# Performance work log

Hardware: AMD Instinct MI355X
Metric: run time of the kernel (lower is better)

The kernel has to match this reference:

```python
import jax, jax.numpy as jnp
import numpy as np

N, E, D, H, O, G = 50000, 640000, 128, 128, 16, 64


def setup_inputs() -> dict:
    key = jax.random.key(0)
    ks = jax.random.split(key, 10)
    x = jax.random.normal(ks[0], (N, D), dtype=jnp.float32)
    edge_index = jax.random.randint(ks[1], (2, E), 0, N, dtype=jnp.int64)
    edge_weight = jax.random.uniform(ks[2], (E,), dtype=jnp.float32)
    batch = jnp.sort(jax.random.randint(ks[3], (N,), 0, G, dtype=jnp.int64))
    s1 = 1.0 / np.sqrt(D)
    s2 = 1.0 / np.sqrt(H)
    W1 = jax.random.uniform(ks[4], (D, H), jnp.float32, -s1, s1)
    b1 = jnp.zeros((H,), jnp.float32)
    W2 = jax.random.uniform(ks[5], (H, H), jnp.float32, -s2, s2)
    b2 = jnp.zeros((H,), jnp.float32)
    Wfc = jax.random.uniform(ks[6], (H, O), jnp.float32, -s2, s2)
    bfc = jax.random.uniform(ks[7], (O,), jnp.float32, -s2, s2)
    return dict(x=x, edge_index=edge_index, edge_weight=edge_weight, batch=batch,
                W1=W1, b1=b1, W2=W2, b2=b2, Wfc=Wfc, bfc=bfc)


def _gcn_conv(x, row, col, ew, W, b, n):
    # PyG GCNConv: out[i] = sum_{(j->i)} norm_ji * (x[j] @ W) + b
    xw = x @ W
    deg = jax.ops.segment_sum(ew, col, num_segments=n)          # [N]
    dinv = jnp.where(deg > 0, jax.lax.rsqrt(deg), 0.0)
    norm = dinv[row] * ew * dinv[col]                           # [E+N]
    msg = xw[row] * norm[:, None]                               # gather + scale
    return jax.ops.segment_sum(msg, col, num_segments=n) + b    # scatter-add


def reference(x, edge_index, edge_weight, batch, W1, b1, W2, b2, Wfc, bfc):
    n = x.shape[0]
    # add self-loops with weight 1 (PyG gcn_norm default)
    loop = jnp.arange(n, dtype=edge_index.dtype)
    row = jnp.concatenate([edge_index[0], loop])
    col = jnp.concatenate([edge_index[1], loop])
    ew = jnp.concatenate([edge_weight, jnp.ones((n,), edge_weight.dtype)])

    h = jax.nn.relu(_gcn_conv(x, row, col, ew, W1, b1, n))
    h = jax.nn.relu(_gcn_conv(h, row, col, ew, W2, b2, n))

    # global_mean_pool over graph ids
    sums = jax.ops.segment_sum(h, batch, num_segments=G)        # [G, H]
    cnt = jax.ops.segment_sum(jnp.ones((n,), h.dtype), batch, num_segments=G)
    pooled = sums / jnp.maximum(cnt, 1.0)[:, None]
    return pooled @ Wfc + bfc                                   # [G, O]
```

## Files before the change

### kernel.cpp

```cpp
#include <hip/hip_runtime.h>


typedef _Float16 h4 __attribute__((ext_vector_type(4)));
typedef _Float16 h8 __attribute__((ext_vector_type(8)));
typedef float f32x4 __attribute__((ext_vector_type(4)));

__global__ void rank_kernel(const int* __restrict__ row, const int* __restrict__ col,
                            int* __restrict__ cnt, unsigned short* __restrict__ rank,
                            int E, int C) {
    int e = blockIdx.x * blockDim.x + threadIdx.x;
    if (e >= E) return;
    int key = col[e] * C + (row[e] >> 13);
    rank[e] = (unsigned short)atomicAdd(&cnt[key], 1);
}

__global__ void block_sum_kernel(const int* __restrict__ cnt, int* __restrict__ bsum, int NC) {
    __shared__ int s[512];
    int t = threadIdx.x;
    int i = blockIdx.x * 512 + t;
    s[t] = (i < NC) ? cnt[i] : 0;
    __syncthreads();
    for (int off = 256; off > 0; off >>= 1) {
        if (t < off) s[t] += s[t + off];
        __syncthreads();
    }
    if (t == 0) bsum[blockIdx.x] = s[0];
}

__global__ void scan_bsum_kernel(const int* __restrict__ bsum, int* __restrict__ boff,
                                 int* __restrict__ rowptr, int NC, int nb) {
    __shared__ int s[1024];
    int t = threadIdx.x;
    int v = (t < nb) ? bsum[t] : 0;
    s[t] = v;
    __syncthreads();
    for (int off = 1; off < 1024; off <<= 1) {
        int u = (t >= off) ? s[t - off] : 0;
        __syncthreads();
        s[t] += u;
        __syncthreads();
    }
    if (t < nb) boff[t] = s[t] - v;
    if (t == nb - 1) rowptr[NC] = s[t];
}

__global__ void rowptr_kernel(const int* __restrict__ cnt, const int* __restrict__ boff,
                              int* __restrict__ rowptr, int NC) {
    __shared__ int s[512];
    int t = threadIdx.x;
    int i = blockIdx.x * 512 + t;
    int v = (i < NC) ? cnt[i] : 0;
    s[t] = v;
    __syncthreads();
    for (int off = 1; off < 512; off <<= 1) {
        int u = (t >= off) ? s[t - off] : 0;
        __syncthreads();
        s[t] += u;
        __syncthreads();
    }
    if (i < NC) rowptr[i] = boff[blockIdx.x] + s[t] - v;
}

__global__ void scatter_kernel(const int* __restrict__ row, const int* __restrict__ col,
                               const float* __restrict__ ew,
                               const unsigned short* __restrict__ rank,
                               const int* __restrict__ rowptr,
                               unsigned int* __restrict__ csr, int E, int C) {
    int e = blockIdx.x * blockDim.x + threadIdx.x;
    if (e >= E) return;
    int r = row[e];
    int pos = rowptr[col[e] * C + (r >> 13)] + (int)rank[e];
    unsigned short hw = __builtin_bit_cast(unsigned short, (_Float16)ew[e]);
    csr[pos] = ((unsigned int)r << 16) | (unsigned int)hw;
}

__global__ __launch_bounds__(256) void deginv_convert_kernel(
        const float4* __restrict__ x4, const unsigned int* __restrict__ csr,
        const int* __restrict__ rowptr, float* __restrict__ dinv,
        h4* __restrict__ p16, int n, int C) {
    int node = blockIdx.x * 8 + (threadIdx.x >> 5);
    if (node >= n) return;
    int lane = threadIdx.x & 31;
    int beg = rowptr[node * C], end = rowptr[node * C + C];
    float sum = 0.0f;
    for (int k = beg + lane; k < end; k += 32) {
        unsigned int v = __builtin_nontemporal_load(csr + k);
        sum += (float)__builtin_bit_cast(_Float16, (unsigned short)(v & 0xffffu));
    }
#pragma unroll
    for (int m = 16; m >= 1; m >>= 1) sum += __shfl_xor(sum, m);
    float di = rsqrtf(1.0f + sum);
    if (lane == 0) dinv[node] = di;
    float4 v = x4[(size_t)node * 32 + lane];
    h4 h;
    h.x = (_Float16)(di * v.x); h.y = (_Float16)(di * v.y);
    h.z = (_Float16)(di * v.z); h.w = (_Float16)(di * v.w);
    p16[(size_t)node * 32 + lane] = h;
}

__global__ __launch_bounds__(256) void agg_kernel(const h4* __restrict__ in16,
                                                  const int* __restrict__ rowptr,
                                                  const unsigned int* __restrict__ csr,
                                                  const float* __restrict__ dinv,
                                                  h4* __restrict__ out16, int n, int C) {
    int node = blockIdx.x * 8 + (threadIdx.x >> 5);
    if (node >= n) return;
    int lane = threadIdx.x & 31;
    float di = dinv[node];
    h4 v = in16[(size_t)node * 32 + lane];
    float ax = (float)v.x, ay = (float)v.y, az = (float)v.z, aw = (float)v.w;
    int beg = rowptr[node * C], end = rowptr[node * C + C];
    int idx = beg;
    for (; idx + 4 <= end; idx += 4) {
        unsigned int e0 = __builtin_nontemporal_load(csr + idx + 0);
        unsigned int e1 = __builtin_nontemporal_load(csr + idx + 1);
        unsigned int e2 = __builtin_nontemporal_load(csr + idx + 2);
        unsigned int e3 = __builtin_nontemporal_load(csr + idx + 3);
        h4 u0 = in16[(size_t)(e0 >> 16) * 32 + lane];
        h4 u1 = in16[(size_t)(e1 >> 16) * 32 + lane];
        h4 u2 = in16[(size_t)(e2 >> 16) * 32 + lane];
        h4 u3 = in16[(size_t)(e3 >> 16) * 32 + lane];
        float w0 = (float)__builtin_bit_cast(_Float16, (unsigned short)(e0 & 0xffffu));
        float w1 = (float)__builtin_bit_cast(_Float16, (unsigned short)(e1 & 0xffffu));
        float w2 = (float)__builtin_bit_cast(_Float16, (unsigned short)(e2 & 0xffffu));
        float w3 = (float)__builtin_bit_cast(_Float16, (unsigned short)(e3 & 0xffffu));
        ax += w0 * (float)u0.x; ay += w0 * (float)u0.y; az += w0 * (float)u0.z; aw += w0 * (float)u0.w;
        ax += w1 * (float)u1.x; ay += w1 * (float)u1.y; az += w1 * (float)u1.z; aw += w1 * (float)u1.w;
        ax += w2 * (float)u2.x; ay += w2 * (float)u2.y; az += w2 * (float)u2.z; aw += w2 * (float)u2.w;
        ax += w3 * (float)u3.x; ay += w3 * (float)u3.y; az += w3 * (float)u3.z; aw += w3 * (float)u3.w;
    }
    for (; idx < end; ++idx) {
        unsigned int e0 = __builtin_nontemporal_load(csr + idx);
        float ww = (float)__builtin_bit_cast(_Float16, (unsigned short)(e0 & 0xffffu));
        h4 u = in16[(size_t)(e0 >> 16) * 32 + lane];
        ax += ww * (float)u.x; ay += ww * (float)u.y;
        az += ww * (float)u.z; aw += ww * (float)u.w;
    }
    h4 r;
    r.x = (_Float16)(ax * di); r.y = (_Float16)(ay * di);
    r.z = (_Float16)(az * di); r.w = (_Float16)(aw * di);
    out16[(size_t)node * 32 + lane] = r;
}

__global__ __launch_bounds__(256) void packW_kernel(const float* __restrict__ W1,
                                                    const float* __restrict__ W2,
                                                    _Float16* __restrict__ Wp1,
                                                    _Float16* __restrict__ Wp2) {
    const float* W = blockIdx.x ? W2 : W1;
    _Float16* Wp = blockIdx.x ? Wp2 : Wp1;
    for (int i = threadIdx.x; i < 2048; i += 256) {
        int lane = i & 63, kc = i >> 6;
        int c = kc >> 2, kb = kc & 3;
        int colq = lane & 15, quad = lane >> 4;
        h8 v;
#pragma unroll
        for (int j = 0; j < 8; ++j)
            v[j] = (_Float16)W[(kb * 32 + quad * 8 + j) * 128 + c * 16 + colq];
        ((h8*)Wp)[i] = v;
    }
}

template <int SCALE>
__global__ __launch_bounds__(256) void gemm_mfma(const _Float16* __restrict__ A,
                                                 const h8* __restrict__ Wp,
                                                 const float* __restrict__ bias,
                                                 const float* __restrict__ dinv,
                                                 _Float16* __restrict__ out16, int n) {
    int wid = threadIdx.x >> 6, lane = threadIdx.x & 63;
    int tb = blockIdx.x * 64 + wid * 16;
    if (tb >= n) return;
    int colq = lane & 15, quad = lane >> 4;

    int arow = tb + colq;
    if (arow >= n) arow = n - 1;
    const h8* Arow = (const h8*)(A + (size_t)arow * 128);
    h8 a[4];
#pragma unroll
    for (int kb = 0; kb < 4; ++kb) a[kb] = Arow[kb * 4 + quad];

    f32x4 acc[8];
#pragma unroll
    for (int c = 0; c < 8; ++c) acc[c] = (f32x4)(0.0f);

#pragma unroll
    for (int c = 0; c < 8; ++c) {
#pragma unroll
        for (int kb = 0; kb < 4; ++kb) {
            h8 b = Wp[(c * 4 + kb) * 64 + lane];
            acc[c] = __builtin_amdgcn_mfma_f32_16x16x32_f16(a[kb], b, acc[c], 0, 0, 0);
        }
    }

#pragma unroll
    for (int c = 0; c < 8; ++c) {
        float bz = bias[c * 16 + colq];
#pragma unroll
        for (int r = 0; r < 4; ++r) {
            int row = tb + quad * 4 + r;
            if (row < n) {
                float v = fmaxf(acc[c][r] + bz, 0.0f);
                if (SCALE) v *= dinv[row];
                out16[(size_t)row * 128 + c * 16 + colq] = (_Float16)v;
            }
        }
    }
}

__global__ __launch_bounds__(256) void poolfc_kernel(const h4* __restrict__ h,
                                                     const int* __restrict__ batch,
                                                     const float* __restrict__ Wfc,
                                                     const float* __restrict__ bfc,
                                                     float* __restrict__ out, int n, int O) {
    int g = blockIdx.x;
    __shared__ int sb[2];
    __shared__ float4 red[256];
    __shared__ float pooled[128];
    int t = threadIdx.x;
    if (t < 2) {
        int target = g + t;
        int lo = 0, hi = n;
        while (lo < hi) { int m = (lo + hi) >> 1; if (batch[m] < target) lo = m + 1; else hi = m; }
        sb[t] = lo;
    }
    __syncthreads();
    int start = sb[0], end = sb[1], len = end - start;
    int gq = t & 31;
    int seg = t >> 5;
    float4 acc; acc.x = acc.y = acc.z = acc.w = 0.0f;
    for (int i = start + seg; i < end; i += 8) {
        h4 v = h[(size_t)i * 32 + gq];
        acc.x += (float)v.x; acc.y += (float)v.y;
        acc.z += (float)v.z; acc.w += (float)v.w;
    }
    red[seg * 32 + gq] = acc;
    __syncthreads();
    if (t < 128) {
        float4 a = red[t], b = red[t + 128];
        a.x += b.x; a.y += b.y; a.z += b.z; a.w += b.w;
        red[t] = a;
    }
    __syncthreads();
    if (t < 64) {
        float4 a = red[t], b = red[t + 64];
        a.x += b.x; a.y += b.y; a.z += b.z; a.w += b.w;
        red[t] = a;
    }
    __syncthreads();
    if (t < 32) {
        float4 a = red[t], b = red[t + 32];
        float inv = (len > 0) ? 1.0f / (float)len : 0.0f;
        pooled[t * 4 + 0] = (a.x + b.x) * inv;
        pooled[t * 4 + 1] = (a.y + b.y) * inv;
        pooled[t * 4 + 2] = (a.z + b.z) * inv;
        pooled[t * 4 + 3] = (a.w + b.w) * inv;
    }
    __syncthreads();
    if (t < O) {
        float a = bfc[t];
        for (int k = 0; k < 128; ++k) a += pooled[k] * Wfc[k * O + t];
        out[g * O + t] = a;
    }
}

extern "C" void kernel_launch(void* const* d_in, const int* in_sizes, int n_in,
                              void* d_out, int out_size, void* d_ws, size_t ws_size,
                              hipStream_t stream) {
    const float* x     = (const float*)d_in[0];
    const int*   ei    = (const int*)d_in[1];
    const float* ew    = (const float*)d_in[2];
    const int*   batch = (const int*)d_in[3];
    const float* W1    = (const float*)d_in[4];
    const float* b1    = (const float*)d_in[5];
    const float* W2    = (const float*)d_in[6];
    const float* b2    = (const float*)d_in[7];
    const float* Wfc   = (const float*)d_in[8];
    const float* bfc   = (const float*)d_in[9];
    float* out = (float*)d_out;

    const int n = in_sizes[0] / 128;
    const int E = in_sizes[2];
    const int O = in_sizes[9];
    const int G = out_size / O;
    const int* row = ei;
    const int* col = ei + E;
    const int C  = (n + 8191) >> 13;
    const int NC = n * C;
    const int NB = (NC + 511) / 512;

    char* p = (char*)d_ws;
    auto alloc = [&](size_t bytes) {
        char* r = p;
        p += (bytes + 255) & ~(size_t)255;
        return r;
    };
    float* dinv    = (float*)alloc((size_t)n * 4);
    int*   cnt     = (int*)alloc((size_t)NC * 4);
    unsigned short* rank = (unsigned short*)alloc((size_t)E * 2);
    int*   rowptr  = (int*)alloc((size_t)(NC + 1) * 4);
    int*   bsum    = (int*)alloc((size_t)NB * 4);
    int*   boff    = (int*)alloc((size_t)NB * 4);
    unsigned int* csr = (unsigned int*)alloc((size_t)E * 4);
    h4*    p1      = (h4*)alloc((size_t)n * 128 * 2);
    h4*    agg16   = (h4*)alloc((size_t)n * 128 * 2);
    h4*    p2      = (h4*)alloc((size_t)n * 128 * 2);
    h4*    h2      = (h4*)alloc((size_t)n * 128 * 2);
    _Float16* Wp1  = (_Float16*)alloc(128 * 128 * 2);
    _Float16* Wp2  = (_Float16*)alloc(128 * 128 * 2);

    hipMemsetAsync(cnt, 0, (size_t)NC * 4, stream);
    packW_kernel<<<2, 256, 0, stream>>>(W1, W2, Wp1, Wp2);
    rank_kernel<<<(E + 255) / 256, 256, 0, stream>>>(row, col, cnt, rank, E, C);
    block_sum_kernel<<<NB, 512, 0, stream>>>(cnt, bsum, NC);
    scan_bsum_kernel<<<1, 1024, 0, stream>>>(bsum, boff, rowptr, NC, NB);
    rowptr_kernel<<<NB, 512, 0, stream>>>(cnt, boff, rowptr, NC);
    scatter_kernel<<<(E + 255) / 256, 256, 0, stream>>>(row, col, ew, rank, rowptr, csr, E, C);
    deginv_convert_kernel<<<(n + 7) / 8, 256, 0, stream>>>((const float4*)x, csr, rowptr, dinv, p1, n, C);

    agg_kernel<<<(n + 7) / 8, 256, 0, stream>>>(p1, rowptr, csr, dinv, agg16, n, C);
    gemm_mfma<1><<<(n + 63) / 64, 256, 0, stream>>>((const _Float16*)agg16, (const h8*)Wp1,
                                                    b1, dinv, (_Float16*)p2, n);

    agg_kernel<<<(n + 7) / 8, 256, 0, stream>>>(p2, rowptr, csr, dinv, agg16, n, C);
    gemm_mfma<0><<<(n + 63) / 64, 256, 0, stream>>>((const _Float16*)agg16, (const h8*)Wp2,
                                                    b2, dinv, (_Float16*)h2, n);

    poolfc_kernel<<<G, 256, 0, stream>>>(h2, batch, Wfc, bfc, out, n, O);
}
```

Before: 267.7 us.

## Drop row-bucketed CSR keys, fuse weight packing, split mean pool across blocks

Builds the CSR keyed only by destination node instead of by (destination, source bucket), which removes the row-bucket sort order and shrinks the count and rowptr arrays by a factor of C. Weight packing is folded into the histogram kernel so one launch does both, and a single memset now clears both the counts and the new pooled buffer. Global mean pooling is split into eight partial blocks per graph that combine with float atomics, followed by a separate small FC kernel that recomputes segment sizes by binary search. The cost is that neighbour lists lose their source-sorted order, which may hurt gather locality in aggregation, and the pooled sums become nondeterministic in order.

After: 254.2 us. 1.05x faster.

```diff
diff --git a/kernel.cpp b/kernel.cpp
--- a/kernel.cpp
+++ b/kernel.cpp
@@ -5,13 +5,28 @@
 typedef _Float16 h8 __attribute__((ext_vector_type(8)));
 typedef float f32x4 __attribute__((ext_vector_type(4)));
 
-__global__ void rank_kernel(const int* __restrict__ row, const int* __restrict__ col,
-                            int* __restrict__ cnt, unsigned short* __restrict__ rank,
-                            int E, int C) {
-    int e = blockIdx.x * blockDim.x + threadIdx.x;
-    if (e >= E) return;
-    int key = col[e] * C + (row[e] >> 13);
-    rank[e] = (unsigned short)atomicAdd(&cnt[key], 1);
+__global__ void hist_pack_kernel(const int* __restrict__ col, int* __restrict__ cnt,
+                                 unsigned short* __restrict__ rank, int E, int NBe,
+                                 const float* __restrict__ W1, const float* __restrict__ W2,
+                                 _Float16* __restrict__ Wp1, _Float16* __restrict__ Wp2) {
+    if (blockIdx.x < (unsigned)NBe) {
+        int e = blockIdx.x * 256 + threadIdx.x;
+        if (e < E) rank[e] = (unsigned short)atomicAdd(&cnt[col[e]], 1);
+        return;
+    }
+    int which = blockIdx.x - NBe;
+    const float* W = which ? W2 : W1;
+    _Float16* Wp = which ? Wp2 : Wp1;
+    for (int i = threadIdx.x; i < 2048; i += 256) {
+        int lane = i & 63, kc = i >> 6;
+        int c = kc >> 2, kb = kc & 3;
+        int colq = lane & 15, quad = lane >> 4;
+        h8 v;
+#pragma unroll
+        for (int j = 0; j < 8; ++j)
+            v[j] = (_Float16)W[(kb * 32 + quad * 8 + j) * 128 + c * 16 + colq];
+        ((h8*)Wp)[i] = v;
+    }
 }
 
 __global__ void block_sum_kernel(const int* __restrict__ cnt, int* __restrict__ bsum, int NC) {
@@ -65,23 +80,22 @@
                                const float* __restrict__ ew,
                                const unsigned short* __restrict__ rank,
                                const int* __restrict__ rowptr,
-                               unsigned int* __restrict__ csr, int E, int C) {
+                               unsigned int* __restrict__ csr, int E) {
     int e = blockIdx.x * blockDim.x + threadIdx.x;
     if (e >= E) return;
-    int r = row[e];
-    int pos = rowptr[col[e] * C + (r >> 13)] + (int)rank[e];
+    int pos = rowptr[col[e]] + (int)rank[e];
     unsigned short hw = __builtin_bit_cast(unsigned short, (_Float16)ew[e]);
-    csr[pos] = ((unsigned int)r << 16) | (unsigned int)hw;
+    csr[pos] = ((unsigned int)row[e] << 16) | (unsigned int)hw;
 }
 
 __global__ __launch_bounds__(256) void deginv_convert_kernel(
         const float4* __restrict__ x4, const unsigned int* __restrict__ csr,
         const int* __restrict__ rowptr, float* __restrict__ dinv,
-        h4* __restrict__ p16, int n, int C) {
+        h4* __restrict__ p16, int n) {
     int node = blockIdx.x * 8 + (threadIdx.x >> 5);
     if (node >= n) return;
     int lane = threadIdx.x & 31;
-    int beg = rowptr[node * C], end = rowptr[node * C + C];
+    int beg = rowptr[node], end = rowptr[node + 1];
     float sum = 0.0f;
     for (int k = beg + lane; k < end; k += 32) {
         unsigned int v = __builtin_nontemporal_load(csr + k);
@@ -102,14 +116,14 @@
                                                   const int* __restrict__ rowptr,
                                                   const unsigned int* __restrict__ csr,
                                                   const float* __restrict__ dinv,
-                                                  h4* __restrict__ out16, int n, int C) {
+                                                  h4* __restrict__ out16, int n) {
     int node = blockIdx.x * 8 + (threadIdx.x >> 5);
     if (node >= n) return;
     int lane = threadIdx.x & 31;
     float di = dinv[node];
     h4 v = in16[(size_t)node * 32 + lane];
     float ax = (float)v.x, ay = (float)v.y, az = (float)v.z, aw = (float)v.w;
-    int beg = rowptr[node * C], end = rowptr[node * C + C];
+    int beg = rowptr[node], end = rowptr[node + 1];
     int idx = beg;
     for (; idx + 4 <= end; idx += 4) {
         unsigned int e0 = __builtin_nontemporal_load(csr + idx + 0);
@@ -142,24 +156,6 @@
     out16[(size_t)node * 32 + lane] = r;
 }
 
-__global__ __launch_bounds__(256) void packW_kernel(const float* __restrict__ W1,
-                                                    const float* __restrict__ W2,
-                                                    _Float16* __restrict__ Wp1,
-                                                    _Float16* __restrict__ Wp2) {
-    const float* W = blockIdx.x ? W2 : W1;
-    _Float16* Wp = blockIdx.x ? Wp2 : Wp1;
-    for (int i = threadIdx.x; i < 2048; i += 256) {
-        int lane = i & 63, kc = i >> 6;
-        int c = kc >> 2, kb = kc & 3;
-        int colq = lane & 15, quad = lane >> 4;
-        h8 v;
-#pragma unroll
-        for (int j = 0; j < 8; ++j)
-            v[j] = (_Float16)W[(kb * 32 + quad * 8 + j) * 128 + c * 16 + colq];
-        ((h8*)Wp)[i] = v;
-    }
-}
-
 template <int SCALE>
 __global__ __launch_bounds__(256) void gemm_mfma(const _Float16* __restrict__ A,
                                                  const h8* __restrict__ Wp,
@@ -206,15 +202,14 @@
     }
 }
 
-__global__ __launch_bounds__(256) void poolfc_kernel(const h4* __restrict__ h,
-                                                     const int* __restrict__ batch,
-                                                     const float* __restrict__ Wfc,
-                                                     const float* __restrict__ bfc,
-                                                     float* __restrict__ out, int n, int O) {
-    int g = blockIdx.x;
+__global__ __launch_bounds__(128) void pool_partial(const h4* __restrict__ h,
+                                                    const int* __restrict__ batch,
+                                                    float* __restrict__ pooled,
+                                                    int n, int splits) {
+    int g = blockIdx.x / splits;
+    int s = blockIdx.x % splits;
     __shared__ int sb[2];
-    __shared__ float4 red[256];
-    __shared__ float pooled[128];
+    __shared__ float4 red[128];
     int t = threadIdx.x;
     if (t < 2) {
         int target = g + t;
@@ -224,42 +219,48 @@
     }
     __syncthreads();
     int start = sb[0], end = sb[1], len = end - start;
+    int a = start + (int)((long long)len * s / splits);
+    int b = start + (int)((long long)len * (s + 1) / splits);
     int gq = t & 31;
     int seg = t >> 5;
     float4 acc; acc.x = acc.y = acc.z = acc.w = 0.0f;
-    for (int i = start + seg; i < end; i += 8) {
+    for (int i = a + seg; i < b; i += 4) {
         h4 v = h[(size_t)i * 32 + gq];
         acc.x += (float)v.x; acc.y += (float)v.y;
         acc.z += (float)v.z; acc.w += (float)v.w;
     }
     red[seg * 32 + gq] = acc;
     __syncthreads();
-    if (t < 128) {
-        float4 a = red[t], b = red[t + 128];
-        a.x += b.x; a.y += b.y; a.z += b.z; a.w += b.w;
-        red[t] = a;
-    }
-    __syncthreads();
     if (t < 64) {
-        float4 a = red[t], b = red[t + 64];
-        a.x += b.x; a.y += b.y; a.z += b.z; a.w += b.w;
-        red[t] = a;
+        float4 u = red[t], w = red[t + 64];
+        u.x += w.x; u.y += w.y; u.z += w.z; u.w += w.w;
+        red[t] = u;
     }
     __syncthreads();
     if (t < 32) {
-        float4 a = red[t], b = red[t + 32];
-        float inv = (len > 0) ? 1.0f / (float)len : 0.0f;
-        pooled[t * 4 + 0] = (a.x + b.x) * inv;
-        pooled[t * 4 + 1] = (a.y + b.y) * inv;
-        pooled[t * 4 + 2] = (a.z + b.z) * inv;
-        pooled[t * 4 + 3] = (a.w + b.w) * inv;
-    }
-    __syncthreads();
-    if (t < O) {
-        float a = bfc[t];
-        for (int k = 0; k < 128; ++k) a += pooled[k] * Wfc[k * O + t];
-        out[g * O + t] = a;
-    }
+        float4 u = red[t], w = red[t + 32];
+        atomicAdd(&pooled[g * 128 + t * 4 + 0], u.x + w.x);
+        atomicAdd(&pooled[g * 128 + t * 4 + 1], u.y + w.y);
+        atomicAdd(&pooled[g * 128 + t * 4 + 2], u.z + w.z);
+        atomicAdd(&pooled[g * 128 + t * 4 + 3], u.w + w.w);
+    }
+}
+
+__global__ void fc_final(const float* __restrict__ pooled, const int* __restrict__ batch,
+                         const float* __restrict__ Wfc, const float* __restrict__ bfc,
+                         float* __restrict__ out, int n, int G, int O) {
+    int gid = blockIdx.x * blockDim.x + threadIdx.x;
+    if (gid >= G * O) return;
+    int g = gid / O, o = gid % O;
+    int lo = 0, hi = n;
+    while (lo < hi) { int m = (lo + hi) >> 1; if (batch[m] < g) lo = m + 1; else hi = m; }
+    int start = lo;
+    lo = 0; hi = n;
+    while (lo < hi) { int m = (lo + hi) >> 1; if (batch[m] < g + 1) lo = m + 1; else hi = m; }
+    float inv = (lo > start) ? 1.0f / (float)(lo - start) : 0.0f;
+    float a = bfc[o];
+    for (int k = 0; k < 128; ++k) a += pooled[g * 128 + k] * inv * Wfc[k * O + o];
+    out[gid] = a;
 }
 
 extern "C" void kernel_launch(void* const* d_in, const int* in_sizes, int n_in,
@@ -283,9 +284,8 @@
     const int G = out_size / O;
     const int* row = ei;
     const int* col = ei + E;
-    const int C  = (n + 8191) >> 13;
-    const int NC = n * C;
-    const int NB = (NC + 511) / 512;
+    const int NB  = (n + 511) / 512;
+    const int NBe = (E + 255) / 256;
 
     char* p = (char*)d_ws;
     auto alloc = [&](size_t bytes) {
@@ -293,10 +293,12 @@
         p += (bytes + 255) & ~(size_t)255;
         return r;
     };
+    int*   cnt     = (int*)alloc((size_t)n * 4);
+    float* pooled  = (float*)alloc((size_t)G * 128 * 4);
+    char*  zend    = p;
     float* dinv    = (float*)alloc((size_t)n * 4);
-    int*   cnt     = (int*)alloc((size_t)NC * 4);
     unsigned short* rank = (unsigned short*)alloc((size_t)E * 2);
-    int*   rowptr  = (int*)alloc((size_t)(NC + 1) * 4);
+    int*   rowptr  = (int*)alloc((size_t)(n + 1) * 4);
     int*   bsum    = (int*)alloc((size_t)NB * 4);
     int*   boff    = (int*)alloc((size_t)NB * 4);
     unsigned int* csr = (unsigned int*)alloc((size_t)E * 4);
@@ -307,22 +309,22 @@
     _Float16* Wp1  = (_Float16*)alloc(128 * 128 * 2);
     _Float16* Wp2  = (_Float16*)alloc(128 * 128 * 2);
 
-    hipMemsetAsync(cnt, 0, (size_t)NC * 4, stream);
-    packW_kernel<<<2, 256, 0, stream>>>(W1, W2, Wp1, Wp2);
-    rank_kernel<<<(E + 255) / 256, 256, 0, stream>>>(row, col, cnt, rank, E, C);
-    block_sum_kernel<<<NB, 512, 0, stream>>>(cnt, bsum, NC);
-    scan_bsum_kernel<<<1, 1024, 0, stream>>>(bsum, boff, rowptr, NC, NB);
-    rowptr_kernel<<<NB, 512, 0, stream>>>(cnt, boff, rowptr, NC);
-    scatter_kernel<<<(E + 255) / 256, 256, 0, stream>>>(row, col, ew, rank, rowptr, csr, E, C);
-    deginv_convert_kernel<<<(n + 7) / 8, 256, 0, stream>>>((const float4*)x, csr, rowptr, dinv, p1, n, C);
-
-    agg_kernel<<<(n + 7) / 8, 256, 0, stream>>>(p1, rowptr, csr, dinv, agg16, n, C);
+    hipMemsetAsync(cnt, 0, (size_t)(zend - (char*)cnt), stream);
+    hist_pack_kernel<<<NBe + 2, 256, 0, stream>>>(col, cnt, rank, E, NBe, W1, W2, Wp1, Wp2);
+    block_sum_kernel<<<NB, 512, 0, stream>>>(cnt, bsum, n);
+    scan_bsum_kernel<<<1, 1024, 0, stream>>>(bsum, boff, rowptr, n, NB);
+    rowptr_kernel<<<NB, 512, 0, stream>>>(cnt, boff, rowptr, n);
+    scatter_kernel<<<NBe, 256, 0, stream>>>(row, col, ew, rank, rowptr, csr, E);
+    deginv_convert_kernel<<<(n + 7) / 8, 256, 0, stream>>>((const float4*)x, csr, rowptr, dinv, p1, n);
+
+    agg_kernel<<<(n + 7) / 8, 256, 0, stream>>>(p1, rowptr, csr, dinv, agg16, n);
     gemm_mfma<1><<<(n + 63) / 64, 256, 0, stream>>>((const _Float16*)agg16, (const h8*)Wp1,
                                                     b1, dinv, (_Float16*)p2, n);
 
-    agg_kernel<<<(n + 7) / 8, 256, 0, stream>>>(p2, rowptr, csr, dinv, agg16, n, C);
+    agg_kernel<<<(n + 7) / 8, 256, 0, stream>>>(p2, rowptr, csr, dinv, agg16, n);
     gemm_mfma<0><<<(n + 63) / 64, 256, 0, stream>>>((const _Float16*)agg16, (const h8*)Wp2,
                                                     b2, dinv, (_Float16*)h2, n);
 
-    poolfc_kernel<<<G, 256, 0, stream>>>(h2, batch, Wfc, bfc, out, n, O);
-}
+    pool_partial<<<G * 8, 128, 0, stream>>>(h2, batch, pooled, n, 8);
+    fc_final<<<(G * O + 255) / 256, 256, 0, stream>>>(pooled, batch, Wfc, bfc, out, n, G, O);
+}
```
